# Kernel tuning notes

Hardware: AMD Instinct MI355X
Metric: run time of the kernel (lower is better)

The kernel has to match this reference:

```python
import jax, jax.numpy as jnp
import numpy as np

Q, B, D, NH, DH, DI, M = 1024, 4, 1024, 16, 64, 4096, 1024
K = Q + M  # klen
SCALE_W = 0.02
LN_EPS = 1e-5


def _layer_norm(x, g, b):
    mu = jnp.mean(x, axis=-1, keepdims=True)
    var = jnp.var(x, axis=-1, keepdims=True)
    return (x - mu) * jax.lax.rsqrt(var + LN_EPS) * g + b


def _rel_shift(x):
    # x: [qlen, klen, bsz, n_head] -> Transformer-XL relative shift
    q, k = x.shape[0], x.shape[1]
    zero_pad = jnp.zeros((q, 1) + x.shape[2:], x.dtype)
    x_padded = jnp.concatenate([zero_pad, x], axis=1)          # [q, k+1, b, n]
    x_padded = x_padded.reshape((k + 1, q) + x.shape[2:])      # [k+1, q, b, n]
    return x_padded[1:].reshape(x.shape)


def setup_inputs() -> dict:
    key = jax.random.key(0)
    ks = jax.random.split(key, 12)
    f32 = jnp.float32
    inp = {
        "w": jax.random.normal(ks[0], (Q, B, D), f32),
        "r": jax.random.normal(ks[1], (K, 1, D), f32),
        "mems": jax.random.normal(ks[2], (M, B, D), f32),
        "qkv_w": SCALE_W * jax.random.normal(ks[3], (D, 3 * NH * DH), f32),
        "r_net_w": SCALE_W * jax.random.normal(ks[4], (D, NH * DH), f32),
        "o_w": SCALE_W * jax.random.normal(ks[5], (NH * DH, D), f32),
        "r_w_bias": SCALE_W * jax.random.normal(ks[6], (NH, DH), f32),
        "r_r_bias": SCALE_W * jax.random.normal(ks[7], (NH, DH), f32),
        "ln1_g": jnp.ones((D,), f32),
        "ln1_b": jnp.zeros((D,), f32),
        "ff_w1": SCALE_W * jax.random.normal(ks[8], (D, DI), f32),
        "ff_b1": jnp.zeros((DI,), f32),
        "ff_w2": SCALE_W * jax.random.normal(ks[9], (DI, D), f32),
        "ff_b2": jnp.zeros((D,), f32),
        "ln2_g": jnp.ones((D,), f32),
        "ln2_b": jnp.zeros((D,), f32),
        # causal mask with memory: query i attends to keys j <= i + mem_len
        "attn_mask": jnp.arange(K)[None, :] > (jnp.arange(Q)[:, None] + M),
    }
    return inp


def reference(w, r, mems, qkv_w, r_net_w, o_w, r_w_bias, r_r_bias,
              ln1_g, ln1_b, ff_w1, ff_b1, ff_w2, ff_b2, ln2_g, ln2_b,
              attn_mask):
    qlen, bsz = w.shape[0], w.shape[1]
    # --- relative multi-head attention (post-lnorm, mems concat) ---
    cat = jnp.concatenate([mems, w], axis=0)                   # [klen, b, d]
    w_heads = cat @ qkv_w                                      # [klen, b, 3*nh*dh]
    r_head_k = (r @ r_net_w).reshape(-1, NH, DH)               # [rlen, nh, dh]
    q_h, k_h, v_h = jnp.split(w_heads, 3, axis=-1)
    klen = k_h.shape[0]
    q_h = q_h[-qlen:].reshape(qlen, bsz, NH, DH)
    k_h = k_h.reshape(klen, bsz, NH, DH)
    v_h = v_h.reshape(klen, bsz, NH, DH)

    rw_q = q_h + r_w_bias[None, None]                          # [q, b, nh, dh]
    AC = jnp.einsum('ibnd,jbnd->ijbn', rw_q, k_h)
    rr_q = q_h + r_r_bias[None, None]
    BD = jnp.einsum('ibnd,jnd->ijbn', rr_q, r_head_k)
    BD = _rel_shift(BD)

    scale = 1.0 / (DH ** 0.5)
    attn_score = (AC + BD) * scale                             # [q, k, b, nh]
    attn_score = jnp.where(attn_mask[:, :, None, None], -jnp.inf, attn_score)
    attn_prob = jax.nn.softmax(attn_score, axis=1)
    attn_vec = jnp.einsum('ijbn,jbnd->ibnd', attn_prob, v_h)
    attn_out = attn_vec.reshape(qlen, bsz, NH * DH) @ o_w      # [q, b, d]
    out = _layer_norm(w + attn_out, ln1_g, ln1_b)

    # --- position-wise FFN (post-lnorm) ---
    core = jax.nn.relu(out @ ff_w1 + ff_b1) @ ff_w2 + ff_b2
    out = _layer_norm(out + core, ln2_g, ln2_b)
    return out
```

## Files before the change

kernel.cpp:

```cpp
#include <hip/hip_runtime.h>
#include <math.h>


#define QLEN 1024
#define BSZ  4
#define DMODEL 1024
#define NHEAD 16
#define DHEAD 64
#define DINNER 4096
#define MEMLEN 1024
#define KLEN 2048

typedef __attribute__((ext_vector_type(8))) short short8;
typedef __attribute__((ext_vector_type(4))) short short4_t;
typedef __attribute__((ext_vector_type(4))) float f32x4;

__device__ __forceinline__ unsigned short f2bf(float x) {
  union { float f; unsigned u; } cv; cv.f = x;
  const unsigned u = cv.u;
  return (unsigned short)((u + 0x7FFFu + ((u >> 16) & 1u)) >> 16);
}
__device__ __forceinline__ float bf2f(unsigned short b) {
  union { unsigned u; float f; } cv; cv.u = ((unsigned)b) << 16;
  return cv.f;
}

__device__ __forceinline__ void gload16(const void* g, void* l) {
  __builtin_amdgcn_global_load_lds(
      (const __attribute__((address_space(1))) unsigned int*)g,
      (__attribute__((address_space(3))) unsigned int*)l, 16, 0, 0);
}

__device__ __forceinline__ int chidx(int row, int kc) {
  return row * 4 + (kc ^ ((row >> 1) & 3));
}

template<int MODE, int TN>
__global__ __launch_bounds__(256) void mgemm(
    const unsigned short* __restrict__ A, const unsigned short* __restrict__ Bt,
    float* __restrict__ C, unsigned short* __restrict__ Cb,
    const float* __restrict__ aux, const float* __restrict__ res,
    unsigned short* __restrict__ oK, unsigned short* __restrict__ oV,
    int Kdim, int N)
{
  __shared__ __align__(16) char smem[8192 + TN * 64];

  const int tid = threadIdx.x;
  const int lane = tid & 63, wv = tid >> 6;
  const int m0 = (int)blockIdx.y * 128, n0 = (int)blockIdx.x * TN;

  const unsigned short *gA0, *gA1, *gB0, *gB1 = nullptr;
  {
    int c = tid, m = c >> 2, kc = (c & 3) ^ ((m >> 1) & 3);
    gA0 = A + (size_t)(m0 + m) * Kdim + kc * 8;
    c = 256 + tid; m = c >> 2; kc = (c & 3) ^ ((m >> 1) & 3);
    gA1 = A + (size_t)(m0 + m) * Kdim + kc * 8;
    c = tid; int nn = c >> 2; kc = (c & 3) ^ ((nn >> 1) & 3);
    gB0 = Bt + (size_t)(n0 + nn) * Kdim + kc * 8;
    if constexpr (TN == 128) {
      c = 256 + tid; nn = c >> 2; kc = (c & 3) ^ ((nn >> 1) & 3);
      gB1 = Bt + (size_t)(n0 + nn) * Kdim + kc * 8;
    }
  }
  char* const lds0 = smem + (tid & 192) * 16;

  const int fr = lane & 15, kq = lane >> 4;
  constexpr int NJ = TN / 32;
  int aoff[4], boff[NJ];
#pragma unroll
  for (int t = 0; t < 4; ++t) {
    const int ra = (wv & 1) * 64 + t * 16 + fr;
    aoff[t] = chidx(ra, kq) * 16;
  }
#pragma unroll
  for (int t = 0; t < NJ; ++t) {
    const int rb = (wv >> 1) * (TN / 2) + t * 16 + fr;
    boff[t] = 8192 + chidx(rb, kq) * 16;
  }

  f32x4 acc[4][NJ] = {};

  for (int k0 = 0; k0 < Kdim; k0 += 32) {
    gload16(gA0, lds0);
    gload16(gA1, lds0 + 4096);
    gload16(gB0, lds0 + 8192);
    if constexpr (TN == 128) gload16(gB1, lds0 + 12288);
    gA0 += 32; gA1 += 32; gB0 += 32;
    if constexpr (TN == 128) gB1 += 32;
    __syncthreads();

    short8 af[4], bf[NJ];
#pragma unroll
    for (int t = 0; t < 4; ++t) af[t] = *(const short8*)(smem + aoff[t]);
#pragma unroll
    for (int t = 0; t < NJ; ++t) bf[t] = *(const short8*)(smem + boff[t]);
#pragma unroll
    for (int i = 0; i < 4; ++i)
#pragma unroll
      for (int j = 0; j < NJ; ++j)
        acc[i][j] = __builtin_amdgcn_mfma_f32_16x16x32_bf16(
            af[i], bf[j], acc[i][j], 0, 0, 0);
    __syncthreads();
  }

  const int rbase = m0 + (wv & 1) * 64 + (lane >> 4) * 4;
  const int cbase = n0 + (wv >> 1) * (TN / 2) + (lane & 15);
#pragma unroll
  for (int i = 0; i < 4; ++i) {
#pragma unroll
    for (int r = 0; r < 4; ++r) {
      const int grow = rbase + i * 16 + r;
#pragma unroll
      for (int j = 0; j < NJ; ++j) {
        const int gcol = cbase + j * 16;
        const float v = acc[i][j][r];
        if constexpr (MODE == 0) {
          const int kkg = grow >> 2, b2 = grow & 3;
          const int sec = gcol >> 10, hn = (gcol >> 6) & 15, d = gcol & 63;
          const unsigned short bv = f2bf(v);
          if (sec == 0) {
            if (kkg >= MEMLEN)
              Cb[((size_t)(b2 * NHEAD + hn) * QLEN + (kkg - MEMLEN)) * DHEAD + d] = bv;
          } else if (sec == 1) {
            oK[((size_t)(b2 * NHEAD + hn) * KLEN + kkg) * DHEAD + d] = bv;
          } else {
            oV[((size_t)(b2 * NHEAD + hn) * KLEN + kkg) * DHEAD + d] = bv;
          }
        } else if constexpr (MODE == 1) {
          const int hn = gcol >> 6, d = gcol & 63;
          Cb[((size_t)hn * KLEN + grow) * DHEAD + d] = f2bf(v);
        } else if constexpr (MODE == 2) {
          C[(size_t)grow * N + gcol] = v + res[(size_t)grow * N + gcol];
        } else if constexpr (MODE == 3) {
          Cb[(size_t)grow * N + gcol] = f2bf(fmaxf(v + aux[gcol], 0.f));
        } else {
          C[(size_t)grow * N + gcol] = v + aux[gcol] + res[(size_t)grow * N + gcol];
        }
      }
    }
  }
}

__global__ __launch_bounds__(256) void transpose_v(
    const unsigned short* __restrict__ Vh, unsigned short* __restrict__ Vt)
{
  __shared__ unsigned short t[64 * 80];
  const int j0 = (int)blockIdx.x * 64;
  const int bn = (int)blockIdx.y;
  const int tid = threadIdx.x;
#pragma unroll
  for (int it = 0; it < 2; ++it) {
    const int f = it * 256 + tid;
    const int j = f >> 3, d8 = (f & 7) * 8;
    const short8 v = *(const short8*)(Vh + ((size_t)bn * KLEN + j0 + j) * DHEAD + d8);
    *(short8*)(t + j * 80 + d8) = v;
  }
  __syncthreads();
  const int d = tid >> 2, jseg = (tid & 3) * 16;
  short8 o0, o1;
#pragma unroll
  for (int e = 0; e < 8; ++e) o0[e] = (short)t[(jseg + e) * 80 + d];
#pragma unroll
  for (int e = 0; e < 8; ++e) o1[e] = (short)t[(jseg + 8 + e) * 80 + d];
  unsigned short* op = Vt + ((size_t)bn * DHEAD + d) * KLEN + j0 + jseg;
  *(short8*)op = o0;
  *(short8*)(op + 8) = o1;
}

__global__ __launch_bounds__(256) void cast_all(
    const float* __restrict__ mems, const float* __restrict__ w,
    const float* __restrict__ r, unsigned short* __restrict__ Xcat,
    unsigned short* __restrict__ Rb16)
{
  const size_t i = ((size_t)blockIdx.x * 256 + threadIdx.x) * 8;
  const float* src;
  unsigned short* dst;
  if (i < 4194304)       { src = mems + i;          dst = Xcat + i; }
  else if (i < 8388608)  { src = w + (i - 4194304); dst = Xcat + i; }
  else                   { src = r + (i - 8388608); dst = Rb16 + (i - 8388608); }
  const float4 x = *(const float4*)src;
  const float4 y = *(const float4*)(src + 4);
  short8 v;
  v[0] = (short)f2bf(x.x); v[1] = (short)f2bf(x.y);
  v[2] = (short)f2bf(x.z); v[3] = (short)f2bf(x.w);
  v[4] = (short)f2bf(y.x); v[5] = (short)f2bf(y.y);
  v[6] = (short)f2bf(y.z); v[7] = (short)f2bf(y.w);
  *(short8*)dst = v;
}

__global__ __launch_bounds__(256) void transpose_all(
    const float* __restrict__ qkv_w, const float* __restrict__ r_net_w,
    const float* __restrict__ o_w, const float* __restrict__ ff_w1,
    const float* __restrict__ ff_w2,
    unsigned short* __restrict__ Wqkv, unsigned short* __restrict__ Wr,
    unsigned short* __restrict__ Wo, unsigned short* __restrict__ W1,
    unsigned short* __restrict__ W2)
{
  const int bid = (int)blockIdx.x;
  const float* in; unsigned short* out; int R, C, xt, loc;
  if (bid < 768)        { in = qkv_w;   out = Wqkv; R = 1024; C = 3072; xt = 48; loc = bid; }
  else if (bid < 1024)  { in = r_net_w; out = Wr;   R = 1024; C = 1024; xt = 16; loc = bid - 768; }
  else if (bid < 1280)  { in = o_w;     out = Wo;   R = 1024; C = 1024; xt = 16; loc = bid - 1024; }
  else if (bid < 2304)  { in = ff_w1;   out = W1;   R = 1024; C = 4096; xt = 64; loc = bid - 1280; }
  else                  { in = ff_w2;   out = W2;   R = 4096; C = 1024; xt = 16; loc = bid - 2304; }
  const int c0 = (loc % xt) * 64, r0 = (loc / xt) * 64;

  __shared__ float t[64][65];
  const int tid = threadIdx.x;
  const int rr = tid >> 4, cc = (tid & 15) * 4;
#pragma unroll
  for (int it = 0; it < 4; ++it) {
    const int rw = rr + it * 16;
    const float4 v = *(const float4*)(in + (size_t)(r0 + rw) * C + c0 + cc);
    t[rw][cc] = v.x; t[rw][cc + 1] = v.y; t[rw][cc + 2] = v.z; t[rw][cc + 3] = v.w;
  }
  __syncthreads();
  const int oc = tid >> 2, ob = (tid & 3) * 16;
#pragma unroll
  for (int j4 = 0; j4 < 4; ++j4) {
    short4_t o;
#pragma unroll
    for (int j = 0; j < 4; ++j) o[j] = (short)f2bf(t[ob + j4 * 4 + j][oc]);
    *(short4_t*)(out + (size_t)(c0 + oc) * R + r0 + ob + j4 * 4) = o;
  }
}

__global__ __launch_bounds__(256, 4) void attn_mfma(
    const unsigned short* __restrict__ Qh, const unsigned short* __restrict__ Kh,
    const unsigned short* __restrict__ Vt, const unsigned short* __restrict__ Rk,
    const float* __restrict__ rwb, const float* __restrict__ rrb,
    float* __restrict__ Opart0, float* __restrict__ Opart1,
    float* __restrict__ den0, float* __restrict__ den1)
{
  __shared__ __align__(16) char smem[40960];
  unsigned short* const Ps = (unsigned short*)(smem + 32768);

  const int tid = threadIdx.x;
  const int lane = tid & 63, wv = tid >> 6;
  const int quad = lane >> 4, l15 = lane & 15;
  const int it = (int)blockIdx.x >> 1, sp = (int)blockIdx.x & 1;
  const int i0 = it * 64;
  const int bn = (int)blockIdx.y, n = bn & 15;

  const int nch = 17 + it;
  const int h = (nch + 1) >> 1;
  const int lo = sp ? h : 0, hi = sp ? nch : h;

  const unsigned short* __restrict__ Qb = Qh + (size_t)bn * QLEN * DHEAD;
  const unsigned short* __restrict__ Kb = Kh + (size_t)bn * KLEN * DHEAD;
  const unsigned short* __restrict__ Vb = Vt + (size_t)bn * DHEAD * KLEN;
  const unsigned short* __restrict__ Rb = Rk + (size_t)n * KLEN * DHEAD;

  short8 qk[2], qr[2];
  {
    const int qrow = i0 + wv * 16 + l15;
    const unsigned short* qp = Qb + (size_t)qrow * DHEAD + quad * 8;
    const float* wp = rwb + n * DHEAD + quad * 8;
    const float* rp = rrb + n * DHEAD + quad * 8;
#pragma unroll
    for (int ks = 0; ks < 2; ++ks) {
      const short8 q8 = *(const short8*)(qp + ks * 32);
#pragma unroll
      for (int e = 0; e < 8; ++e) {
        const float qv = bf2f((unsigned short)q8[e]);
        qk[ks][e] = (short)f2bf(qv + wp[ks * 32 + e]);
        qr[ks][e] = (short)f2bf(qv + rp[ks * 32 + e]);
      }
    }
  }

  int srcl[4];
  bool condE[4];
#pragma unroll
  for (int r = 0; r < 4; ++r) {
    const int E = l15 - quad * 4 - r + 15;
    srcl[r] = (lane & 48) | (E & 15);
    condE[r] = (E >= 16);
  }

  f32x4 O[4] = {};
  float rden[4] = {0.f, 0.f, 0.f, 0.f};
  char* const lds0 = smem + (tid & 192) * 16;

  for (int ch = lo; ch < hi; ++ch) {
    const int j0 = ch * 64;
    const int gw = j0 - i0 + 960;

    __syncthreads();

#pragma unroll
    for (int t2 = 0; t2 < 2; ++t2) {
      const int s = t2 * 256 + tid;
      const int row = s >> 3, kc = (s & 7) ^ (row & 7);
      gload16(Kb + (((size_t)(j0 + row)) << 6) + kc * 8, lds0 + t2 * 4096);
    }
#pragma unroll
    for (int t2 = 0; t2 < 2; ++t2) {
      const int s = t2 * 256 + tid;
      const int row = s >> 3, kc = (s & 7) ^ (row & 7);
      gload16(Vb + (((size_t)row) << 11) + j0 + kc * 8, lds0 + 8192 + t2 * 4096);
    }
    if (ch == lo) {
#pragma unroll
      for (int t2 = 0; t2 < 4; ++t2) {
        const int rr = t2 * 32 + (tid >> 3);
        const int gr = gw + rr;
        const int kc = (tid & 7) ^ (rr & 7);
        const int pb = ((gw + t2 * 32) & 127) * 128;
        gload16(Rb + (((size_t)gr) << 6) + kc * 8,
                smem + 16384 + pb + (tid & 192) * 16);
      }
    } else {
#pragma unroll
      for (int t2 = 0; t2 < 2; ++t2) {
        const int rr = t2 * 32 + (tid >> 3);
        const int gr = gw + 64 + rr;
        const int kc = (tid & 7) ^ (rr & 7);
        const int pb = ((gw + 64 + t2 * 32) & 127) * 128;
        gload16(Rb + (((size_t)gr) << 6) + kc * 8,
                smem + 16384 + pb + (tid & 192) * 16);
      }
    }
    __syncthreads();

    f32x4 sk[4];
#pragma unroll
    for (int jt = 0; jt < 4; ++jt) {
      f32x4 a = {0.f, 0.f, 0.f, 0.f};
#pragma unroll
      for (int ks = 0; ks < 2; ++ks) {
        const int frr = jt * 16 + l15;
        const int c = (ks * 4 + quad) ^ (l15 & 7);
        const short8 kf = *(const short8*)(smem + (frr * 8 + c) * 16);
        a = __builtin_amdgcn_mfma_f32_16x16x32_bf16(qk[ks], kf, a, 0, 0, 0);
      }
      sk[jt] = a;
    }
    f32x4 uu[5];
#pragma unroll
    for (int s = 0; s < 5; ++s) {
      f32x4 a = {0.f, 0.f, 0.f, 0.f};
      const int frr = (gw + (3 - wv + s) * 16 + l15) & 127;
#pragma unroll
      for (int ks = 0; ks < 2; ++ks) {
        const int c = (ks * 4 + quad) ^ (l15 & 7);
        const short8 rf = *(const short8*)(smem + 16384 + (frr * 8 + c) * 16);
        a = __builtin_amdgcn_mfma_f32_16x16x32_bf16(qr[ks], rf, a, 0, 0, 0);
      }
      uu[s] = a;
    }

    float rot[5][4];
#pragma unroll
    for (int s = 0; s < 5; ++s)
#pragma unroll
      for (int r = 0; r < 4; ++r)
        rot[s][r] = __shfl(uu[s][r], srcl[r], 64);

#pragma unroll
    for (int jt = 0; jt < 4; ++jt) {
      const int jl = jt * 16 + l15;
#pragma unroll
      for (int r = 0; r < 4; ++r) {
        const int il = wv * 16 + quad * 4 + r;
        const int dj = (j0 + jl) - (i0 + il);
        const float uv = condE[r] ? rot[jt + 1][r] : rot[jt][r];
        const float sv = (sk[jt][r] + uv) * 0.125f;
        const float p = (dj <= 1024) ? __expf(sv) : 0.f;
        rden[r] += p;
        Ps[(il * 8 + ((jl >> 3) ^ (il & 7))) * 8 + (jl & 7)] = f2bf(p);
      }
    }

#pragma unroll
    for (int ks = 0; ks < 2; ++ks) {
      const int frp = wv * 16 + l15;
      const int cp = (ks * 4 + quad) ^ (l15 & 7);
      const short8 pf = *(const short8*)(smem + 32768 + (frp * 8 + cp) * 16);
#pragma unroll
      for (int dt = 0; dt < 4; ++dt) {
        const int vr = dt * 16 + l15;
        const short8 vf = *(const short8*)(smem + 8192 + (vr * 8 + cp) * 16);
        O[dt] = __builtin_amdgcn_mfma_f32_16x16x32_bf16(pf, vf, O[dt], 0, 0, 0);
      }
    }
  }

#pragma unroll
  for (int m = 1; m < 16; m <<= 1)
#pragma unroll
    for (int r = 0; r < 4; ++r)
      rden[r] += __shfl_xor(rden[r], m, 64);

  float* const Op = sp ? Opart1 : Opart0;
  float* const dp = sp ? den1 : den0;
  const size_t ob = (size_t)(bn * 16 + it) * 64;
#pragma unroll
  for (int r = 0; r < 4; ++r) {
    const int il = wv * 16 + quad * 4 + r;
#pragma unroll
    for (int dt = 0; dt < 4; ++dt)
      Op[(ob + il) * 64 + dt * 16 + l15] = O[dt][r];
    if (l15 == 0) dp[ob + il] = rden[r];
  }
}

__global__ __launch_bounds__(256) void attn_combine(
    const float* __restrict__ O0, const float* __restrict__ O1,
    const float* __restrict__ d0, const float* __restrict__ d1,
    unsigned short* __restrict__ AVb)
{
  const int blk = (int)blockIdx.x;
  const int bn = blk >> 4, it = blk & 15;
  const int b = bn >> 4, n = bn & 15;
  const int tid = threadIdx.x;
  const int il = tid >> 2, ds = (tid & 3) * 16;
  const size_t base = ((size_t)blk * 64 + il) * 64 + ds;
  const float inv = 1.f / (d0[blk * 64 + il] + d1[blk * 64 + il]);
  short8 o0, o1;
#pragma unroll
  for (int g = 0; g < 2; ++g) {
    const float4 a = *(const float4*)(O0 + base + g * 8);
    const float4 bb = *(const float4*)(O1 + base + g * 8);
    const float4 a2 = *(const float4*)(O0 + base + g * 8 + 4);
    const float4 b2 = *(const float4*)(O1 + base + g * 8 + 4);
    short8& o = g ? o1 : o0;
    o[0] = (short)f2bf((a.x + bb.x) * inv);  o[1] = (short)f2bf((a.y + bb.y) * inv);
    o[2] = (short)f2bf((a.z + bb.z) * inv);  o[3] = (short)f2bf((a.w + bb.w) * inv);
    o[4] = (short)f2bf((a2.x + b2.x) * inv); o[5] = (short)f2bf((a2.y + b2.y) * inv);
    o[6] = (short)f2bf((a2.z + b2.z) * inv); o[7] = (short)f2bf((a2.w + b2.w) * inv);
  }
  unsigned short* op =
      AVb + ((size_t)(it * 64 + il) * BSZ + b) * DMODEL + n * DHEAD + ds;
  *(short8*)op = o0;
  *(short8*)(op + 8) = o1;
}

__global__ __launch_bounds__(256) void ln_kernel(
    float* __restrict__ X, const float* __restrict__ gw,
    const float* __restrict__ bw, unsigned short* __restrict__ bfo)
{
  const int row = blockIdx.x, tid = threadIdx.x;
  float* rp = X + (size_t)row * DMODEL;
  const float4 x = *(const float4*)(rp + tid * 4);
  float s = x.x + x.y + x.z + x.w;
  float q = x.x * x.x + x.y * x.y + x.z * x.z + x.w * x.w;
#pragma unroll
  for (int m = 1; m < 64; m <<= 1) {
    s += __shfl_xor(s, m, 64);
    q += __shfl_xor(q, m, 64);
  }
  __shared__ float ss[4], sq[4];
  if ((tid & 63) == 0) { ss[tid >> 6] = s; sq[tid >> 6] = q; }
  __syncthreads();
  s = ss[0] + ss[1] + ss[2] + ss[3];
  q = sq[0] + sq[1] + sq[2] + sq[3];
  const float mu = s * (1.f / DMODEL);
  const float var = q * (1.f / DMODEL) - mu * mu;
  const float rstd = rsqrtf(var + 1e-5f);
  const float4 g4 = *(const float4*)(gw + tid * 4);
  const float4 b4 = *(const float4*)(bw + tid * 4);
  float4 y;
  y.x = (x.x - mu) * rstd * g4.x + b4.x;
  y.y = (x.y - mu) * rstd * g4.y + b4.y;
  y.z = (x.z - mu) * rstd * g4.z + b4.z;
  y.w = (x.w - mu) * rstd * g4.w + b4.w;
  *(float4*)(rp + tid * 4) = y;
  if (bfo) {
    short4_t o;
    o[0] = (short)f2bf(y.x); o[1] = (short)f2bf(y.y);
    o[2] = (short)f2bf(y.z); o[3] = (short)f2bf(y.w);
    *(short4_t*)(bfo + (size_t)row * DMODEL + tid * 4) = o;
  }
}

extern "C" void kernel_launch(void* const* d_in, const int* in_sizes, int n_in,
                              void* d_out, int out_size, void* d_ws,
                              size_t ws_size, hipStream_t stream)
{
  const float* w       = (const float*)d_in[0];
  const float* r       = (const float*)d_in[1];
  const float* mems    = (const float*)d_in[2];
  const float* qkv_w   = (const float*)d_in[3];
  const float* r_net_w = (const float*)d_in[4];
  const float* o_w     = (const float*)d_in[5];
  const float* r_w_bias= (const float*)d_in[6];
  const float* r_r_bias= (const float*)d_in[7];
  const float* ln1_g   = (const float*)d_in[8];
  const float* ln1_b   = (const float*)d_in[9];
  const float* ff_w1   = (const float*)d_in[10];
  const float* ff_b1   = (const float*)d_in[11];
  const float* ff_w2   = (const float*)d_in[12];
  const float* ff_b2   = (const float*)d_in[13];
  const float* ln2_g   = (const float*)d_in[14];
  const float* ln2_b   = (const float*)d_in[15];
  float* out = (float*)d_out;

  float* X1 = (float*)d_ws;
  unsigned short* Qh   = (unsigned short*)(X1 + 4194304);
  unsigned short* Kh   = Qh + 4194304;
  unsigned short* Vt   = Kh + 8388608;
  unsigned short* Rk   = Vt + 8388608;
  unsigned short* Xcat = Rk + 2097152 + 8192;
  unsigned short* Wqkv = Xcat + 8388608;
  unsigned short* Wr   = Wqkv + 3145728;
  unsigned short* Wo   = Wr + 1048576;
  unsigned short* W1   = Wo + 1048576;
  unsigned short* W2   = W1 + 4194304;
  float* den0 = (float*)(W2 + 4194304);
  float* den1 = den0 + 65536;
  unsigned short* AVb  = (unsigned short*)(den1 + 65536);
  unsigned short* Vh     = (unsigned short*)X1;
  unsigned short* Rb16   = AVb;
  float* Opart0          = (float*)X1;
  float* Opart1          = (float*)Xcat;
  unsigned short* X1b    = Qh;
  unsigned short* H      = Kh;

  const dim3 blk(256);

  cast_all<<<dim3(5120), blk, 0, stream>>>(mems, w, r, Xcat, Rb16);
  transpose_all<<<dim3(3328), blk, 0, stream>>>(
      qkv_w, r_net_w, o_w, ff_w1, ff_w2, Wqkv, Wr, Wo, W1, W2);

  mgemm<0, 128><<<dim3(24, 64), blk, 0, stream>>>(
      Xcat, Wqkv, nullptr, Qh, nullptr, nullptr, Kh, Vh, DMODEL, 3 * DMODEL);
  transpose_v<<<dim3(32, 64), blk, 0, stream>>>(Vh, Vt);
  mgemm<1, 64><<<dim3(16, 16), blk, 0, stream>>>(
      Rb16, Wr, nullptr, Rk, nullptr, nullptr, nullptr, nullptr, DMODEL, DMODEL);
  attn_mfma<<<dim3(32, 64), blk, 0, stream>>>(
      Qh, Kh, Vt, Rk, r_w_bias, r_r_bias, Opart0, Opart1, den0, den1);
  attn_combine<<<dim3(1024), blk, 0, stream>>>(Opart0, Opart1, den0, den1, AVb);
  mgemm<2, 64><<<dim3(16, 32), blk, 0, stream>>>(
      AVb, Wo, X1, nullptr, nullptr, w, nullptr, nullptr, DMODEL, DMODEL);
  ln_kernel<<<dim3(4096), blk, 0, stream>>>(X1, ln1_g, ln1_b, X1b);
  mgemm<3, 128><<<dim3(32, 32), blk, 0, stream>>>(
      X1b, W1, nullptr, H, ff_b1, nullptr, nullptr, nullptr, DMODEL, DINNER);
  mgemm<4, 64><<<dim3(16, 32), blk, 0, stream>>>(
      H, W2, out, nullptr, ff_b2, X1, nullptr, nullptr, DINNER, DMODEL);
  ln_kernel<<<dim3(4096), blk, 0, stream>>>(out, ln2_g, ln2_b, nullptr);

  (void)in_sizes; (void)n_in; (void)out_size; (void)ws_size;
}
```

Before: 615.2 us.

## Double-buffer K/V/R tiles in attention kernel and remap block-to-head schedule

New measurement: 559.0 us. 9.1% less time.

```diff
diff --git a/kernel.cpp b/kernel.cpp
--- a/kernel.cpp
+++ b/kernel.cpp
@@ -225,22 +225,26 @@
   }
 }
 
-__global__ __launch_bounds__(256, 4) void attn_mfma(
+__global__ __launch_bounds__(256, 2) void attn_mfma(
     const unsigned short* __restrict__ Qh, const unsigned short* __restrict__ Kh,
     const unsigned short* __restrict__ Vt, const unsigned short* __restrict__ Rk,
     const float* __restrict__ rwb, const float* __restrict__ rrb,
     float* __restrict__ Opart0, float* __restrict__ Opart1,
     float* __restrict__ den0, float* __restrict__ den1)
 {
-  __shared__ __align__(16) char smem[40960];
-  unsigned short* const Ps = (unsigned short*)(smem + 32768);
+  __shared__ __align__(16) char smem[65536];
 
   const int tid = threadIdx.x;
   const int lane = tid & 63, wv = tid >> 6;
   const int quad = lane >> 4, l15 = lane & 15;
-  const int it = (int)blockIdx.x >> 1, sp = (int)blockIdx.x & 1;
+
+  const int bid0 = (int)blockIdx.y * 32 + (int)blockIdx.x;
+  const int slot = bid0 >> 3;
+  const int bn = (bid0 & 7) * 8 + (slot >> 5);
+  const int inner = slot & 31;
+  const int it = inner >> 1, sp = inner & 1;
   const int i0 = it * 64;
-  const int bn = (int)blockIdx.y, n = bn & 15;
+  const int n = bn & 15;
 
   const int nch = 17 + it;
   const int h = (nch + 1) >> 1;
@@ -280,48 +284,82 @@
 
   f32x4 O[4] = {};
   float rden[4] = {0.f, 0.f, 0.f, 0.f};
-  char* const lds0 = smem + (tid & 192) * 16;
-
-  for (int ch = lo; ch < hi; ++ch) {
-    const int j0 = ch * 64;
-    const int gw = j0 - i0 + 960;
-
-    __syncthreads();
-
+  const int wvoff = (tid & 192) * 16;
+
+  {
+    const int j0 = lo * 64;
+    const int g64 = lo - it + 15;
+    const int rb3 = (g64 % 3) * 64;
 #pragma unroll
     for (int t2 = 0; t2 < 2; ++t2) {
       const int s = t2 * 256 + tid;
       const int row = s >> 3, kc = (s & 7) ^ (row & 7);
-      gload16(Kb + (((size_t)(j0 + row)) << 6) + kc * 8, lds0 + t2 * 4096);
+      gload16(Kb + (((size_t)(j0 + row)) << 6) + kc * 8,
+              smem + t2 * 4096 + wvoff);
     }
 #pragma unroll
     for (int t2 = 0; t2 < 2; ++t2) {
       const int s = t2 * 256 + tid;
       const int row = s >> 3, kc = (s & 7) ^ (row & 7);
-      gload16(Vb + (((size_t)row) << 11) + j0 + kc * 8, lds0 + 8192 + t2 * 4096);
-    }
-    if (ch == lo) {
-#pragma unroll
-      for (int t2 = 0; t2 < 4; ++t2) {
-        const int rr = t2 * 32 + (tid >> 3);
-        const int gr = gw + rr;
-        const int kc = (tid & 7) ^ (rr & 7);
-        const int pb = ((gw + t2 * 32) & 127) * 128;
-        gload16(Rb + (((size_t)gr) << 6) + kc * 8,
-                smem + 16384 + pb + (tid & 192) * 16);
-      }
-    } else {
+      gload16(Vb + (((size_t)row) << 11) + j0 + kc * 8,
+              smem + 16384 + t2 * 4096 + wvoff);
+    }
+    const int gw = j0 - i0 + 960;
+#pragma unroll
+    for (int t2 = 0; t2 < 4; ++t2) {
+      const int rr = t2 * 32 + (tid >> 3);
+      const int gr = gw + rr;
+      const int kc = (tid & 7) ^ (rr & 7);
+      int pb = rb3 + t2 * 32; if (pb >= 192) pb -= 192;
+      gload16(Rb + (((size_t)gr) << 6) + kc * 8,
+              smem + 32768 + pb * 128 + wvoff);
+    }
+  }
+
+  int cur = 0;
+  for (int ch = lo; ch < hi; ++ch) {
+    const int j0 = ch * 64;
+    const int g64 = ch - it + 15;
+    const int rb3 = (g64 % 3) * 64;
+    const int gw = j0 - i0 + 960;
+
+    asm volatile("s_waitcnt lgkmcnt(0)" ::: "memory");
+    __builtin_amdgcn_s_barrier();
+
+    if (ch + 1 < hi) {
+      const int nb = cur ^ 1;
+      const int j0n = j0 + 64;
+#pragma unroll
+      for (int t2 = 0; t2 < 2; ++t2) {
+        const int s = t2 * 256 + tid;
+        const int row = s >> 3, kc = (s & 7) ^ (row & 7);
+        gload16(Kb + (((size_t)(j0n + row)) << 6) + kc * 8,
+                smem + nb * 8192 + t2 * 4096 + wvoff);
+      }
+#pragma unroll
+      for (int t2 = 0; t2 < 2; ++t2) {
+        const int s = t2 * 256 + tid;
+        const int row = s >> 3, kc = (s & 7) ^ (row & 7);
+        gload16(Vb + (((size_t)row) << 11) + j0n + kc * 8,
+                smem + 16384 + nb * 8192 + t2 * 4096 + wvoff);
+      }
 #pragma unroll
       for (int t2 = 0; t2 < 2; ++t2) {
         const int rr = t2 * 32 + (tid >> 3);
-        const int gr = gw + 64 + rr;
+        const int gr = gw + 128 + rr;
         const int kc = (tid & 7) ^ (rr & 7);
-        const int pb = ((gw + 64 + t2 * 32) & 127) * 128;
+        int pb = rb3 + 128 + t2 * 32; if (pb >= 192) pb -= 192;
         gload16(Rb + (((size_t)gr) << 6) + kc * 8,
-                smem + 16384 + pb + (tid & 192) * 16);
-      }
-    }
-    __syncthreads();
+                smem + 32768 + pb * 128 + wvoff);
+      }
+      asm volatile("s_waitcnt vmcnt(6)" ::: "memory");
+    } else {
+      asm volatile("s_waitcnt vmcnt(0)" ::: "memory");
+    }
+    __builtin_amdgcn_s_barrier();
+
+    const char* const kbase = smem + cur * 8192;
+    const char* const vbase = smem + 16384 + cur * 8192;
 
     f32x4 sk[4];
 #pragma unroll
@@ -331,7 +369,7 @@
       for (int ks = 0; ks < 2; ++ks) {
         const int frr = jt * 16 + l15;
         const int c = (ks * 4 + quad) ^ (l15 & 7);
-        const short8 kf = *(const short8*)(smem + (frr * 8 + c) * 16);
+        const short8 kf = *(const short8*)(kbase + (frr * 8 + c) * 16);
         a = __builtin_amdgcn_mfma_f32_16x16x32_bf16(qk[ks], kf, a, 0, 0, 0);
       }
       sk[jt] = a;
@@ -340,11 +378,12 @@
 #pragma unroll
     for (int s = 0; s < 5; ++s) {
       f32x4 a = {0.f, 0.f, 0.f, 0.f};
-      const int frr = (gw + (3 - wv + s) * 16 + l15) & 127;
+      int frr = rb3 + (3 - wv + s) * 16 + l15;
+      if (frr >= 192) frr -= 192;
 #pragma unroll
       for (int ks = 0; ks < 2; ++ks) {
         const int c = (ks * 4 + quad) ^ (l15 & 7);
-        const short8 rf = *(const short8*)(smem + 16384 + (frr * 8 + c) * 16);
+        const short8 rf = *(const short8*)(smem + 32768 + (frr * 8 + c) * 16);
         a = __builtin_amdgcn_mfma_f32_16x16x32_bf16(qr[ks], rf, a, 0, 0, 0);
       }
       uu[s] = a;
@@ -357,6 +396,7 @@
       for (int r = 0; r < 4; ++r)
         rot[s][r] = __shfl(uu[s][r], srcl[r], 64);
 
+    unsigned short* const Ps = (unsigned short*)(smem + 57344);
 #pragma unroll
     for (int jt = 0; jt < 4; ++jt) {
       const int jl = jt * 16 + l15;
@@ -376,14 +416,15 @@
     for (int ks = 0; ks < 2; ++ks) {
       const int frp = wv * 16 + l15;
       const int cp = (ks * 4 + quad) ^ (l15 & 7);
-      const short8 pf = *(const short8*)(smem + 32768 + (frp * 8 + cp) * 16);
+      const short8 pf = *(const short8*)(smem + 57344 + (frp * 8 + cp) * 16);
 #pragma unroll
       for (int dt = 0; dt < 4; ++dt) {
         const int vr = dt * 16 + l15;
-        const short8 vf = *(const short8*)(smem + 8192 + (vr * 8 + cp) * 16);
+        const short8 vf = *(const short8*)(vbase + (vr * 8 + cp) * 16);
         O[dt] = __builtin_amdgcn_mfma_f32_16x16x32_bf16(pf, vf, O[dt], 0, 0, 0);
       }
     }
+    cur ^= 1;
   }
 
 #pragma unroll
```
